# Optimization experiments

Measured on AMD Instinct MI355X. Metric: run time of the kernel, lower is better.

Reference implementation:

```python
import jax, jax.numpy as jnp
import numpy as np

B, N, E = 4, 10000, 160000
NODE_DIM, EDGE_DIM, HIDDEN, HEADS = 128, 64, 256, 8
HEAD_DIM = HIDDEN // HEADS
LN_EPS = 1e-5


def setup_inputs() -> dict:
    key = jax.random.key(0)
    ks = jax.random.split(key, 11)
    s = 0.05  # stand-in for xavier scale
    return {
        "node_feat": jax.random.normal(ks[0], (B, N, NODE_DIM), dtype=jnp.float32),
        "edge_index": jax.random.randint(ks[1], (2, E), 0, N, dtype=jnp.int64),
        "edge_attr": jax.random.normal(ks[2], (B, E, EDGE_DIM), dtype=jnp.float32),
        "W_node": jax.random.normal(ks[3], (NODE_DIM, HIDDEN), dtype=jnp.float32) * s,
        "W_edge": jax.random.normal(ks[4], (EDGE_DIM, HIDDEN), dtype=jnp.float32) * s,
        "W_res": jax.random.normal(ks[5], (NODE_DIM, HIDDEN), dtype=jnp.float32) * s,
        "att_src": jax.random.normal(ks[6], (HEADS, HEAD_DIM), dtype=jnp.float32) * s,
        "att_dst": jax.random.normal(ks[7], (HEADS, HEAD_DIM), dtype=jnp.float32) * s,
        "att_edge": jax.random.normal(ks[8], (HEADS, HEAD_DIM), dtype=jnp.float32) * s,
        "ln_gamma": jnp.ones((HIDDEN,), dtype=jnp.float32),
        "ln_beta": jnp.zeros((HIDDEN,), dtype=jnp.float32),
    }


def reference(node_feat, edge_index, edge_attr, W_node, W_edge, W_res,
              att_src, att_dst, att_edge, ln_gamma, ln_beta):
    b, n, _ = node_feat.shape
    e_cnt = edge_attr.shape[1]
    src = edge_index[0]
    dst = edge_index[1]

    h = (node_feat @ W_node).reshape(b, n, HEADS, HEAD_DIM)          # [B,N,H,D]
    e = (edge_attr @ W_edge).reshape(b, e_cnt, HEADS, HEAD_DIM)       # [B,E,H,D]
    h_src = h[:, src]                                                 # [B,E,H,D]
    h_dst = h[:, dst]                                                 # [B,E,H,D]

    logits = (jnp.einsum('behd,hd->beh', h_src, att_src)
              + jnp.einsum('behd,hd->beh', h_dst, att_dst)
              + jnp.einsum('behd,hd->beh', e, att_edge))              # [B,E,H]
    logits = jax.nn.leaky_relu(logits, negative_slope=0.2)

    # segment softmax over edges grouped by dst node (edge-leading layout)
    lt = logits.transpose(1, 0, 2)                                    # [E,B,H]
    seg_max = jax.ops.segment_max(lt, dst, num_segments=n)            # [N,B,H]
    ex = jnp.exp(lt - seg_max[dst])
    seg_sum = jax.ops.segment_sum(ex, dst, num_segments=n)            # [N,B,H]
    alpha = ex / seg_sum[dst]                                         # [E,B,H]

    msg = alpha[..., None] * (h_src + e).transpose(1, 0, 2, 3)        # [E,B,H,D]
    agg = jax.ops.segment_sum(msg, dst, num_segments=n)               # [N,B,H,D]
    out = agg.transpose(1, 0, 2, 3).reshape(b, n, HIDDEN)             # [B,N,HIDDEN]

    x = out + node_feat @ W_res
    mu = jnp.mean(x, axis=-1, keepdims=True)
    var = jnp.mean(jnp.square(x - mu), axis=-1, keepdims=True)
    x = (x - mu) * jax.lax.rsqrt(var + LN_EPS) * ln_gamma + ln_beta
    return jax.nn.elu(x)
```

## Files before the change

### kernel.cpp

```cpp
#include <hip/hip_runtime.h>

#define BB 4
#define NN 10000
#define EE 160000
#define HID 256
#define NHEAD 8

typedef __attribute__((ext_vector_type(8))) short short8v;
typedef __attribute__((ext_vector_type(4))) float f32x4;

__device__ __forceinline__ unsigned short f2bf(float f) {
  unsigned u = __float_as_uint(f);
  unsigned r = (u + 0x7fffu + ((u >> 16) & 1u)) >> 16;
  return (unsigned short)r;
}

__global__ void k_prep(const float* __restrict__ We, const float* __restrict__ ae,
                       float* __restrict__ What) {
  int t = threadIdx.x;
  int k = t >> 3, hh = t & 7;
  float s = 0.f;
#pragma unroll
  for (int d = 0; d < 32; ++d) s += We[k * HID + hh * 32 + d] * ae[hh * 32 + d];
  What[k * NHEAD + hh] = s;
}

__global__ __launch_bounds__(256) void k_cvt(const float* __restrict__ nf,
                                             unsigned short* __restrict__ nf16) {
  const int g = blockIdx.x * 256 + threadIdx.x;
  const float4* s = reinterpret_cast<const float4*>(nf) + (size_t)g * 2;
  const float4 a = s[0], b = s[1];
  short8v v;
  v[0] = f2bf(a.x); v[1] = f2bf(a.y); v[2] = f2bf(a.z); v[3] = f2bf(a.w);
  v[4] = f2bf(b.x); v[5] = f2bf(b.y); v[6] = f2bf(b.z); v[7] = f2bf(b.w);
  *reinterpret_cast<short8v*>(nf16 + (size_t)g * 8) = v;
}

__global__ __launch_bounds__(256) void k_pack(const float* __restrict__ Wn,
                                              const float* __restrict__ Wr,
                                              unsigned short* __restrict__ Bpack) {
  const int nt = blockIdx.x;
  const int ks = threadIdx.x >> 6;
  const int l = threadIdx.x & 63;
  const int col = nt * 16 + (l & 15);
  const int k0 = ks * 32 + (l >> 4) * 8;
  const float* __restrict__ src = (nt < 16) ? Wn : Wr;
  const int c2 = col & 255;
  short8v v;
#pragma unroll
  for (int e = 0; e < 8; ++e) v[e] = f2bf(src[(k0 + e) * HID + c2]);
  *reinterpret_cast<short8v*>(Bpack + ((size_t)(nt * 4 + ks) * 64 + l) * 8) = v;
}

__global__ __launch_bounds__(512) void k_projm(
    const unsigned short* __restrict__ nf16,
    const unsigned short* __restrict__ Bpack,
    float* __restrict__ h, float* __restrict__ res) {
  const int t = threadIdx.x;
  const int w = t >> 6, l = t & 63;
  const int base = blockIdx.x * 64 + (w & 3) * 16;
  const int nhalf = w >> 2;
  short8v a[4];
#pragma unroll
  for (int ks = 0; ks < 4; ++ks)
    a[ks] = *reinterpret_cast<const short8v*>(
        nf16 + (size_t)(base + (l & 15)) * 128 + ks * 32 + (l >> 4) * 8);
  f32x4 acc[16];
#pragma unroll
  for (int i = 0; i < 16; ++i) acc[i] = (f32x4){0.f, 0.f, 0.f, 0.f};
  const short8v* bp =
      reinterpret_cast<const short8v*>(Bpack) + (size_t)nhalf * 4096 + l;
#pragma unroll
  for (int nt = 0; nt < 16; ++nt) {
#pragma unroll
    for (int ks = 0; ks < 4; ++ks) {
      const short8v bf = bp[(nt * 4 + ks) * 64];
      acc[nt] = __builtin_amdgcn_mfma_f32_16x16x32_bf16(a[ks], bf, acc[nt], 0, 0, 0);
    }
  }
  float* __restrict__ outp = nhalf ? res : h;
#pragma unroll
  for (int nt = 0; nt < 16; ++nt) {
    const int col = nt * 16 + (l & 15);
#pragma unroll
    for (int b = 0; b < 4; ++b) {
      const int row = base + (l >> 4) * 4 + b;
      outp[(size_t)row * HID + col] = acc[nt][b];
    }
  }
}

__global__ __launch_bounds__(256) void k_att(
    const float* __restrict__ h, const float* __restrict__ as_,
    const float* __restrict__ ad_, float* __restrict__ ssrc,
    float* __restrict__ sdst) {
  const int w = threadIdx.x >> 6, l = threadIdx.x & 63;
  const size_t bn = (size_t)blockIdx.x * 4 + w;
  const float4 hv = reinterpret_cast<const float4*>(h + bn * HID)[l];
  const float4 av = reinterpret_cast<const float4*>(as_)[l];
  const float4 dv = reinterpret_cast<const float4*>(ad_)[l];
  float ps = hv.x * av.x + hv.y * av.y + hv.z * av.z + hv.w * av.w;
  float pd = hv.x * dv.x + hv.y * dv.y + hv.z * dv.z + hv.w * dv.w;
#pragma unroll
  for (int off = 1; off <= 4; off <<= 1) {
    ps += __shfl_xor(ps, off);
    pd += __shfl_xor(pd, off);
  }
  if ((l & 7) == 0) {
    ssrc[bn * NHEAD + (l >> 3)] = ps;
    sdst[bn * NHEAD + (l >> 3)] = pd;
  }
}

__global__ __launch_bounds__(256) void k_elogit(
    const float* __restrict__ ea, const int* __restrict__ ei,
    const float* __restrict__ What, const float* __restrict__ ssrc,
    const float* __restrict__ sdst, float* __restrict__ logits) {
  __shared__ float sea[32 * 65];
  __shared__ float sw[64 * NHEAD];
  const int t = threadIdx.x;
  sw[t] = What[t];
  sw[t + 256] = What[t + 256];
  const int g0 = blockIdx.x * 32;
  const float* base = ea + (size_t)g0 * 64;
#pragma unroll
  for (int j = 0; j < 8; ++j) {
    int f = t + j * 256;
    sea[(f >> 6) * 65 + (f & 63)] = base[f];
  }
  __syncthreads();
  const int il = t >> 3, hh = t & 7;
  const int g = g0 + il;
  float acc = 0.f;
#pragma unroll
  for (int k = 0; k < 64; ++k) acc += sea[il * 65 + k] * sw[k * NHEAD + hh];
  const int b = g / EE, e = g - b * EE;
  const int src = ei[e], dst = ei[EE + e];
  float lg = ssrc[((size_t)b * NN + src) * NHEAD + hh] +
             sdst[((size_t)b * NN + dst) * NHEAD + hh] + acc;
  lg = lg > 0.f ? lg : 0.2f * lg;
  logits[(size_t)g * NHEAD + hh] = lg;
}

__global__ void k_hist(const int* __restrict__ ei, int* __restrict__ cnt) {
  int e = blockIdx.x * 256 + threadIdx.x;
  if (e < EE) atomicAdd(&cnt[ei[EE + e]], 1);
}

__global__ __launch_bounds__(1024) void k_scan(const int* __restrict__ cnt,
                                               int* __restrict__ off) {
  __shared__ int ls[1024];
  const int t = threadIdx.x;
  int own = 0;
  int deg[10];
  if (t < 1000) {
#pragma unroll
    for (int i = 0; i < 10; ++i) { deg[i] = cnt[t * 10 + i]; own += deg[i]; }
  }
  ls[t] = own;
  __syncthreads();
  for (int s = 1; s < 1024; s <<= 1) {
    int v = 0;
    if (t >= s) v = ls[t - s];
    __syncthreads();
    if (t >= s) ls[t] += v;
    __syncthreads();
  }
  if (t < 1000) {
    int start = ls[t] - own;
#pragma unroll
    for (int i = 0; i < 10; ++i) { off[t * 10 + i] = start; start += deg[i]; }
  }
  if (t == 0) off[NN] = EE;
}

__global__ void k_scatter(const int* __restrict__ ei, const int* __restrict__ off,
                          int* __restrict__ cur, int* __restrict__ perm,
                          int* __restrict__ esrc) {
  int e = blockIdx.x * 256 + threadIdx.x;
  if (e >= EE) return;
  int d = ei[EE + e];
  int pos = off[d] + atomicAdd(&cur[d], 1);
  perm[pos] = e;
  esrc[pos] = ei[e];
}

__global__ __launch_bounds__(256) void k_agg(
    const float* __restrict__ ea, const float* __restrict__ h,
    const float* __restrict__ logits, const int* __restrict__ off,
    const int* __restrict__ perm, const int* __restrict__ esrc,
    const float* __restrict__ We, const float* __restrict__ res,
    const float* __restrict__ gam, const float* __restrict__ bet,
    float* __restrict__ out) {
  __shared__ float zsh[4][8 * 65];
  const int wid = threadIdx.x >> 6, l = threadIdx.x & 63;
  const int b = wid, node = blockIdx.x;
  const int start = off[node], end = off[node + 1];
  const int hq = l >> 3;
  const int hr = l & 7;
  float m = -3.0e38f;
  for (int i = start + (l >> 3); i < end; i += 8) {
    int e = perm[i];
    m = fmaxf(m, logits[((size_t)b * EE + e) * 8 + hr]);
  }
  m = fmaxf(m, __shfl_xor(m, 8));
  m = fmaxf(m, __shfl_xor(m, 16));
  m = fmaxf(m, __shfl_xor(m, 32));
  float4 u4 = {0.f, 0.f, 0.f, 0.f};
  float z0 = 0.f, z1 = 0.f, z2 = 0.f, z3 = 0.f;
  float z4 = 0.f, z5 = 0.f, z6 = 0.f, z7 = 0.f;
  float ss = 0.f;
  for (int i = start; i < end; ++i) {
    const int e = perm[i];
    const int src = esrc[i];
    const float lg = logits[((size_t)b * EE + e) * 8 + hr];
    const float exl = __expf(lg - m);
    ss += exl;
    const float eal = ea[((size_t)b * EE + e) * 64 + l];
    const float e0 = __shfl(exl, 0), e1 = __shfl(exl, 1);
    const float e2 = __shfl(exl, 2), e3 = __shfl(exl, 3);
    const float e4 = __shfl(exl, 4), e5 = __shfl(exl, 5);
    const float e6 = __shfl(exl, 6), e7 = __shfl(exl, 7);
    z0 += e0 * eal; z1 += e1 * eal; z2 += e2 * eal; z3 += e3 * eal;
    z4 += e4 * eal; z5 += e5 * eal; z6 += e6 * eal; z7 += e7 * eal;
    const float exu = __shfl(exl, hq);
    const float4 hs =
        *reinterpret_cast<const float4*>(h + (((size_t)b * NN + src) << 8) + 4 * l);
    u4.x += exu * hs.x; u4.y += exu * hs.y;
    u4.z += exu * hs.z; u4.w += exu * hs.w;
  }
  zsh[wid][0 * 65 + l] = z0; zsh[wid][1 * 65 + l] = z1;
  zsh[wid][2 * 65 + l] = z2; zsh[wid][3 * 65 + l] = z3;
  zsh[wid][4 * 65 + l] = z4; zsh[wid][5 * 65 + l] = z5;
  zsh[wid][6 * 65 + l] = z6; zsh[wid][7 * 65 + l] = z7;
  const float4* We4 = reinterpret_cast<const float4*>(We);
  const float4 r4 =
      *reinterpret_cast<const float4*>(res + (((size_t)b * NN + node) << 8) + 4 * l);
#pragma unroll 8
  for (int k = 0; k < 64; ++k) {
    const float zk = zsh[wid][hq * 65 + k];
    const float4 wv = We4[k * 64 + l];
    u4.x += zk * wv.x; u4.y += zk * wv.y;
    u4.z += zk * wv.z; u4.w += zk * wv.w;
  }
  const float ssq = __shfl(ss, hq);
  const float sc = ssq > 0.f ? 1.f / ssq : 0.f;
  u4.x = u4.x * sc + r4.x; u4.y = u4.y * sc + r4.y;
  u4.z = u4.z * sc + r4.z; u4.w = u4.w * sc + r4.w;
  float s1 = u4.x + u4.y + u4.z + u4.w;
  float s2 = u4.x * u4.x + u4.y * u4.y + u4.z * u4.z + u4.w * u4.w;
#pragma unroll
  for (int off2 = 1; off2 <= 32; off2 <<= 1) {
    s1 += __shfl_xor(s1, off2);
    s2 += __shfl_xor(s2, off2);
  }
  const float mu = s1 * (1.f / HID);
  const float var = s2 * (1.f / HID) - mu * mu;
  const float rstd = rsqrtf(var + 1e-5f);
  const float4 g4 = reinterpret_cast<const float4*>(gam)[l];
  const float4 b4 = reinterpret_cast<const float4*>(bet)[l];
  float4 y;
  y.x = (u4.x - mu) * rstd * g4.x + b4.x;
  y.y = (u4.y - mu) * rstd * g4.y + b4.y;
  y.z = (u4.z - mu) * rstd * g4.z + b4.z;
  y.w = (u4.w - mu) * rstd * g4.w + b4.w;
  y.x = y.x > 0.f ? y.x : expm1f(y.x);
  y.y = y.y > 0.f ? y.y : expm1f(y.y);
  y.z = y.z > 0.f ? y.z : expm1f(y.z);
  y.w = y.w > 0.f ? y.w : expm1f(y.w);
  *reinterpret_cast<float4*>(out + (((size_t)b * NN + node) << 8) + 4 * l) = y;
}

extern "C" void kernel_launch(void* const* d_in, const int* in_sizes, int n_in,
                              void* d_out, int out_size, void* d_ws, size_t ws_size,
                              hipStream_t stream) {
  const float* nf   = (const float*)d_in[0];
  const int*   ei   = (const int*)d_in[1];
  const float* eatt = (const float*)d_in[2];
  const float* Wn   = (const float*)d_in[3];
  const float* We   = (const float*)d_in[4];
  const float* Wr   = (const float*)d_in[5];
  const float* as_  = (const float*)d_in[6];
  const float* ad_  = (const float*)d_in[7];
  const float* ae_  = (const float*)d_in[8];
  const float* gam  = (const float*)d_in[9];
  const float* bet  = (const float*)d_in[10];
  float* out = (float*)d_out;

  char* ws = (char*)d_ws;
  size_t off_b = 0;
  float* h      = (float*)(ws + off_b); off_b += (size_t)BB * NN * HID * 4;
  float* ssrc   = (float*)(ws + off_b); size_t csr_off = off_b; off_b += (size_t)BB * NN * NHEAD * 4;
  float* sdst   = (float*)(ws + off_b); off_b += (size_t)BB * NN * NHEAD * 4;
  float* What   = (float*)(ws + off_b); off_b += 64 * NHEAD * 4;
  size_t logits_off = off_b;
  float* logits = (float*)(ws + off_b); off_b += (size_t)BB * EE * NHEAD * 4;
  float* res    = (float*)(ws + off_b); off_b += (size_t)BB * NN * HID * 4;
  unsigned short* nf16  = (unsigned short*)(ws + logits_off);
  unsigned short* Bpack = (unsigned short*)(ws + logits_off + ((size_t)12 << 20));
  char* csr = ws + csr_off;
  int* cnt  = (int*)(csr);
  int* offn = (int*)(csr + 40 * 1024);
  int* cur  = (int*)(csr + 2 * 40 * 1024);
  int* perm = (int*)(csr + 3 * 40 * 1024);
  int* esrc = (int*)(csr + 3 * 40 * 1024 + (size_t)EE * 4);

  hipLaunchKernelGGL(k_prep, dim3(1), dim3(512), 0, stream, We, ae_, What);
  hipLaunchKernelGGL(k_cvt, dim3(2500), dim3(256), 0, stream, nf, nf16);
  hipLaunchKernelGGL(k_pack, dim3(32), dim3(256), 0, stream, Wn, Wr, Bpack);
  hipLaunchKernelGGL(k_projm, dim3(BB * NN / 64), dim3(512), 0, stream,
                     nf16, Bpack, h, res);
  hipLaunchKernelGGL(k_att, dim3(BB * NN / 4), dim3(256), 0, stream,
                     h, as_, ad_, ssrc, sdst);
  hipLaunchKernelGGL(k_elogit, dim3(BB * EE / 32), dim3(256), 0, stream,
                     eatt, ei, What, ssrc, sdst, logits);
  hipMemsetAsync(csr, 0, 3 * 40 * 1024, stream);
  hipLaunchKernelGGL(k_hist, dim3((EE + 255) / 256), dim3(256), 0, stream, ei, cnt);
  hipLaunchKernelGGL(k_scan, dim3(1), dim3(1024), 0, stream, cnt, offn);
  hipLaunchKernelGGL(k_scatter, dim3((EE + 255) / 256), dim3(256), 0, stream,
                     ei, offn, cur, perm, esrc);
  hipLaunchKernelGGL(k_agg, dim3(NN), dim3(256), 0, stream,
                     eatt, h, logits, offn, perm, esrc, We, res, gam, bet, out);
}
```

Measured before the change: 302.2 us.

## Store h in bf16, precompute CSR-ordered exp logits with atomic segment max

```diff
diff --git a/kernel.cpp b/kernel.cpp
--- a/kernel.cpp
+++ b/kernel.cpp
@@ -13,6 +13,16 @@
   unsigned u = __float_as_uint(f);
   unsigned r = (u + 0x7fffu + ((u >> 16) & 1u)) >> 16;
   return (unsigned short)r;
+}
+__device__ __forceinline__ float bf2f(unsigned short u) {
+  return __uint_as_float(((unsigned)u) << 16);
+}
+__device__ __forceinline__ unsigned fenc(float f) {
+  unsigned u = __float_as_uint(f);
+  return (u & 0x80000000u) ? ~u : (u | 0x80000000u);
+}
+__device__ __forceinline__ float fdec(unsigned u) {
+  return __uint_as_float((u & 0x80000000u) ? (u ^ 0x80000000u) : ~u);
 }
 
 __global__ void k_prep(const float* __restrict__ We, const float* __restrict__ ae,
@@ -55,7 +65,7 @@
 __global__ __launch_bounds__(512) void k_projm(
     const unsigned short* __restrict__ nf16,
     const unsigned short* __restrict__ Bpack,
-    float* __restrict__ h, float* __restrict__ res) {
+    unsigned short* __restrict__ h16, float* __restrict__ res) {
   const int t = threadIdx.x;
   const int w = t >> 6, l = t & 63;
   const int base = blockIdx.x * 64 + (w & 3) * 16;
@@ -78,29 +88,30 @@
       acc[nt] = __builtin_amdgcn_mfma_f32_16x16x32_bf16(a[ks], bf, acc[nt], 0, 0, 0);
     }
   }
-  float* __restrict__ outp = nhalf ? res : h;
 #pragma unroll
   for (int nt = 0; nt < 16; ++nt) {
     const int col = nt * 16 + (l & 15);
 #pragma unroll
     for (int b = 0; b < 4; ++b) {
       const int row = base + (l >> 4) * 4 + b;
-      outp[(size_t)row * HID + col] = acc[nt][b];
+      if (nhalf == 0) h16[(size_t)row * HID + col] = f2bf(acc[nt][b]);
+      else            res[(size_t)row * HID + col] = acc[nt][b];
     }
   }
 }
 
 __global__ __launch_bounds__(256) void k_att(
-    const float* __restrict__ h, const float* __restrict__ as_,
+    const unsigned short* __restrict__ h16, const float* __restrict__ as_,
     const float* __restrict__ ad_, float* __restrict__ ssrc,
     float* __restrict__ sdst) {
   const int w = threadIdx.x >> 6, l = threadIdx.x & 63;
   const size_t bn = (size_t)blockIdx.x * 4 + w;
-  const float4 hv = reinterpret_cast<const float4*>(h + bn * HID)[l];
+  const ushort4 hv = *reinterpret_cast<const ushort4*>(h16 + bn * HID + 4 * l);
   const float4 av = reinterpret_cast<const float4*>(as_)[l];
   const float4 dv = reinterpret_cast<const float4*>(ad_)[l];
-  float ps = hv.x * av.x + hv.y * av.y + hv.z * av.z + hv.w * av.w;
-  float pd = hv.x * dv.x + hv.y * dv.y + hv.z * dv.z + hv.w * dv.w;
+  const float x0 = bf2f(hv.x), x1 = bf2f(hv.y), x2 = bf2f(hv.z), x3 = bf2f(hv.w);
+  float ps = x0 * av.x + x1 * av.y + x2 * av.z + x3 * av.w;
+  float pd = x0 * dv.x + x1 * dv.y + x2 * dv.z + x3 * dv.w;
 #pragma unroll
   for (int off = 1; off <= 4; off <<= 1) {
     ps += __shfl_xor(ps, off);
@@ -110,36 +121,6 @@
     ssrc[bn * NHEAD + (l >> 3)] = ps;
     sdst[bn * NHEAD + (l >> 3)] = pd;
   }
-}
-
-__global__ __launch_bounds__(256) void k_elogit(
-    const float* __restrict__ ea, const int* __restrict__ ei,
-    const float* __restrict__ What, const float* __restrict__ ssrc,
-    const float* __restrict__ sdst, float* __restrict__ logits) {
-  __shared__ float sea[32 * 65];
-  __shared__ float sw[64 * NHEAD];
-  const int t = threadIdx.x;
-  sw[t] = What[t];
-  sw[t + 256] = What[t + 256];
-  const int g0 = blockIdx.x * 32;
-  const float* base = ea + (size_t)g0 * 64;
-#pragma unroll
-  for (int j = 0; j < 8; ++j) {
-    int f = t + j * 256;
-    sea[(f >> 6) * 65 + (f & 63)] = base[f];
-  }
-  __syncthreads();
-  const int il = t >> 3, hh = t & 7;
-  const int g = g0 + il;
-  float acc = 0.f;
-#pragma unroll
-  for (int k = 0; k < 64; ++k) acc += sea[il * 65 + k] * sw[k * NHEAD + hh];
-  const int b = g / EE, e = g - b * EE;
-  const int src = ei[e], dst = ei[EE + e];
-  float lg = ssrc[((size_t)b * NN + src) * NHEAD + hh] +
-             sdst[((size_t)b * NN + dst) * NHEAD + hh] + acc;
-  lg = lg > 0.f ? lg : 0.2f * lg;
-  logits[(size_t)g * NHEAD + hh] = lg;
 }
 
 __global__ void k_hist(const int* __restrict__ ei, int* __restrict__ cnt) {
@@ -175,59 +156,94 @@
 }
 
 __global__ void k_scatter(const int* __restrict__ ei, const int* __restrict__ off,
-                          int* __restrict__ cur, int* __restrict__ perm,
-                          int* __restrict__ esrc) {
+                          int* __restrict__ cur, int2* __restrict__ eidx,
+                          int* __restrict__ inv, int* __restrict__ edst) {
   int e = blockIdx.x * 256 + threadIdx.x;
   if (e >= EE) return;
-  int d = ei[EE + e];
+  int s = ei[e], d = ei[EE + e];
   int pos = off[d] + atomicAdd(&cur[d], 1);
-  perm[pos] = e;
-  esrc[pos] = ei[e];
+  eidx[pos] = make_int2(e, s);
+  inv[e] = pos;
+  edst[pos] = d;
+}
+
+__global__ __launch_bounds__(256) void k_elogit(
+    const float* __restrict__ ea, const int* __restrict__ ei,
+    const float* __restrict__ What, const float* __restrict__ ssrc,
+    const float* __restrict__ sdst, const int* __restrict__ inv,
+    float* __restrict__ logitsP, unsigned* __restrict__ smax) {
+  __shared__ float sea[32 * 65];
+  __shared__ float sw[64 * NHEAD];
+  const int t = threadIdx.x;
+  sw[t] = What[t];
+  sw[t + 256] = What[t + 256];
+  const int g0 = blockIdx.x * 32;
+  const float* base = ea + (size_t)g0 * 64;
+#pragma unroll
+  for (int j = 0; j < 8; ++j) {
+    int f = t + j * 256;
+    sea[(f >> 6) * 65 + (f & 63)] = base[f];
+  }
+  __syncthreads();
+  const int il = t >> 3, hh = t & 7;
+  const int g = g0 + il;
+  float acc = 0.f;
+#pragma unroll
+  for (int k = 0; k < 64; ++k) acc += sea[il * 65 + k] * sw[k * NHEAD + hh];
+  const int b = g / EE, e = g - b * EE;
+  const int src = ei[e], dst = ei[EE + e];
+  float lg = ssrc[((size_t)b * NN + src) * NHEAD + hh] +
+             sdst[((size_t)b * NN + dst) * NHEAD + hh] + acc;
+  lg = lg > 0.f ? lg : 0.2f * lg;
+  const int pos = inv[e];
+  logitsP[((size_t)b * EE + pos) * 8 + hh] = lg;
+  atomicMax(&smax[((size_t)b * NN + dst) * 8 + hh], fenc(lg));
+}
+
+__global__ __launch_bounds__(256) void k_ex(float* __restrict__ exP,
+                                            const int* __restrict__ edst,
+                                            const unsigned* __restrict__ smax) {
+  const size_t t = (size_t)blockIdx.x * 256 + threadIdx.x;
+  const int g = (int)(t >> 3), hh = (int)(t & 7);
+  const int b = g / EE, i = g - b * EE;
+  const int d = edst[i];
+  const float mx = fdec(smax[((size_t)b * NN + d) * 8 + hh]);
+  exP[t] = __expf(exP[t] - mx);
 }
 
 __global__ __launch_bounds__(256) void k_agg(
-    const float* __restrict__ ea, const float* __restrict__ h,
-    const float* __restrict__ logits, const int* __restrict__ off,
-    const int* __restrict__ perm, const int* __restrict__ esrc,
-    const float* __restrict__ We, const float* __restrict__ res,
-    const float* __restrict__ gam, const float* __restrict__ bet,
-    float* __restrict__ out) {
+    const float* __restrict__ ea, const unsigned short* __restrict__ h16,
+    const float* __restrict__ exP, const int* __restrict__ off,
+    const int2* __restrict__ eidx, const float* __restrict__ We,
+    const float* __restrict__ res, const float* __restrict__ gam,
+    const float* __restrict__ bet, float* __restrict__ out) {
   __shared__ float zsh[4][8 * 65];
   const int wid = threadIdx.x >> 6, l = threadIdx.x & 63;
   const int b = wid, node = blockIdx.x;
   const int start = off[node], end = off[node + 1];
   const int hq = l >> 3;
   const int hr = l & 7;
-  float m = -3.0e38f;
-  for (int i = start + (l >> 3); i < end; i += 8) {
-    int e = perm[i];
-    m = fmaxf(m, logits[((size_t)b * EE + e) * 8 + hr]);
-  }
-  m = fmaxf(m, __shfl_xor(m, 8));
-  m = fmaxf(m, __shfl_xor(m, 16));
-  m = fmaxf(m, __shfl_xor(m, 32));
   float4 u4 = {0.f, 0.f, 0.f, 0.f};
   float z0 = 0.f, z1 = 0.f, z2 = 0.f, z3 = 0.f;
   float z4 = 0.f, z5 = 0.f, z6 = 0.f, z7 = 0.f;
   float ss = 0.f;
+  const float* __restrict__ exb = exP + (size_t)b * EE * 8;
+  const float* __restrict__ eab = ea + (size_t)b * EE * 64;
+  const unsigned short* __restrict__ hb = h16 + (size_t)b * NN * 256;
+#pragma unroll 2
   for (int i = start; i < end; ++i) {
-    const int e = perm[i];
-    const int src = esrc[i];
-    const float lg = logits[((size_t)b * EE + e) * 8 + hr];
-    const float exl = __expf(lg - m);
-    ss += exl;
-    const float eal = ea[((size_t)b * EE + e) * 64 + l];
-    const float e0 = __shfl(exl, 0), e1 = __shfl(exl, 1);
-    const float e2 = __shfl(exl, 2), e3 = __shfl(exl, 3);
-    const float e4 = __shfl(exl, 4), e5 = __shfl(exl, 5);
-    const float e6 = __shfl(exl, 6), e7 = __shfl(exl, 7);
-    z0 += e0 * eal; z1 += e1 * eal; z2 += e2 * eal; z3 += e3 * eal;
-    z4 += e4 * eal; z5 += e5 * eal; z6 += e6 * eal; z7 += e7 * eal;
-    const float exu = __shfl(exl, hq);
-    const float4 hs =
-        *reinterpret_cast<const float4*>(h + (((size_t)b * NN + src) << 8) + 4 * l);
-    u4.x += exu * hs.x; u4.y += exu * hs.y;
-    u4.z += exu * hs.z; u4.w += exu * hs.w;
+    const int2 es = eidx[i];
+    const float4 xa = *reinterpret_cast<const float4*>(exb + (size_t)i * 8);
+    const float4 xb = *reinterpret_cast<const float4*>(exb + (size_t)i * 8 + 4);
+    const float exu = exb[(size_t)i * 8 + hq];
+    ss += exb[(size_t)i * 8 + hr];
+    const float eal = eab[(size_t)es.x * 64 + l];
+    const ushort4 h4 =
+        *reinterpret_cast<const ushort4*>(hb + (size_t)es.y * 256 + 4 * l);
+    z0 += xa.x * eal; z1 += xa.y * eal; z2 += xa.z * eal; z3 += xa.w * eal;
+    z4 += xb.x * eal; z5 += xb.y * eal; z6 += xb.z * eal; z7 += xb.w * eal;
+    u4.x += exu * bf2f(h4.x); u4.y += exu * bf2f(h4.y);
+    u4.z += exu * bf2f(h4.z); u4.w += exu * bf2f(h4.w);
   }
   zsh[wid][0 * 65 + l] = z0; zsh[wid][1 * 65 + l] = z1;
   zsh[wid][2 * 65 + l] = z2; zsh[wid][3 * 65 + l] = z3;
@@ -288,37 +304,48 @@
   float* out = (float*)d_out;
 
   char* ws = (char*)d_ws;
-  size_t off_b = 0;
-  float* h      = (float*)(ws + off_b); off_b += (size_t)BB * NN * HID * 4;
-  float* ssrc   = (float*)(ws + off_b); size_t csr_off = off_b; off_b += (size_t)BB * NN * NHEAD * 4;
-  float* sdst   = (float*)(ws + off_b); off_b += (size_t)BB * NN * NHEAD * 4;
-  float* What   = (float*)(ws + off_b); off_b += 64 * NHEAD * 4;
-  size_t logits_off = off_b;
-  float* logits = (float*)(ws + off_b); off_b += (size_t)BB * EE * NHEAD * 4;
-  float* res    = (float*)(ws + off_b); off_b += (size_t)BB * NN * HID * 4;
-  unsigned short* nf16  = (unsigned short*)(ws + logits_off);
-  unsigned short* Bpack = (unsigned short*)(ws + logits_off + ((size_t)12 << 20));
-  char* csr = ws + csr_off;
-  int* cnt  = (int*)(csr);
-  int* offn = (int*)(csr + 40 * 1024);
-  int* cur  = (int*)(csr + 2 * 40 * 1024);
-  int* perm = (int*)(csr + 3 * 40 * 1024);
-  int* esrc = (int*)(csr + 3 * 40 * 1024 + (size_t)EE * 4);
+  size_t o = 0;
+  auto alloc = [&](size_t bytes) -> void* {
+    void* p = ws + o;
+    o += (bytes + 255) & ~(size_t)255;
+    return p;
+  };
+  unsigned short* h16 = (unsigned short*)alloc((size_t)BB * NN * HID * 2);
+  float* ssrc    = (float*)alloc((size_t)BB * NN * NHEAD * 4);
+  float* sdst    = (float*)alloc((size_t)BB * NN * NHEAD * 4);
+  float* What    = (float*)alloc(64 * NHEAD * 4);
+  float* logitsP = (float*)alloc((size_t)BB * EE * NHEAD * 4);
+  float* res     = (float*)alloc((size_t)BB * NN * HID * 4);
+  int*  cnt      = (int*)alloc(NN * 4);
+  int*  cur      = (int*)alloc(NN * 4);
+  int*  offn     = (int*)alloc((NN + 1) * 4);
+  int2* eidx     = (int2*)alloc((size_t)EE * 8);
+
+  char* ob = (char*)d_out;
+  unsigned short* nf16  = (unsigned short*)ob;
+  unsigned short* Bpack = (unsigned short*)(ob + ((size_t)12 << 20));
+  unsigned* smax = (unsigned*)(ob + ((size_t)16 << 20));
+  int* inv       = (int*)(ob + ((size_t)18 << 20));
+  int* edst      = (int*)(ob + ((size_t)20 << 20));
 
   hipLaunchKernelGGL(k_prep, dim3(1), dim3(512), 0, stream, We, ae_, What);
   hipLaunchKernelGGL(k_cvt, dim3(2500), dim3(256), 0, stream, nf, nf16);
   hipLaunchKernelGGL(k_pack, dim3(32), dim3(256), 0, stream, Wn, Wr, Bpack);
   hipLaunchKernelGGL(k_projm, dim3(BB * NN / 64), dim3(512), 0, stream,
-                     nf16, Bpack, h, res);
+                     nf16, Bpack, h16, res);
   hipLaunchKernelGGL(k_att, dim3(BB * NN / 4), dim3(256), 0, stream,
-                     h, as_, ad_, ssrc, sdst);
-  hipLaunchKernelGGL(k_elogit, dim3(BB * EE / 32), dim3(256), 0, stream,
-                     eatt, ei, What, ssrc, sdst, logits);
-  hipMemsetAsync(csr, 0, 3 * 40 * 1024, stream);
+                     h16, as_, ad_, ssrc, sdst);
+  hipMemsetAsync(cnt, 0, NN * 4, stream);
+  hipMemsetAsync(cur, 0, NN * 4, stream);
+  hipMemsetAsync(smax, 0, (size_t)BB * NN * NHEAD * 4, stream);
   hipLaunchKernelGGL(k_hist, dim3((EE + 255) / 256), dim3(256), 0, stream, ei, cnt);
   hipLaunchKernelGGL(k_scan, dim3(1), dim3(1024), 0, stream, cnt, offn);
   hipLaunchKernelGGL(k_scatter, dim3((EE + 255) / 256), dim3(256), 0, stream,
-                     ei, offn, cur, perm, esrc);
+                     ei, offn, cur, eidx, inv, edst);
+  hipLaunchKernelGGL(k_elogit, dim3(BB * EE / 32), dim3(256), 0, stream,
+                     eatt, ei, What, ssrc, sdst, inv, logitsP, smax);
+  hipLaunchKernelGGL(k_ex, dim3((size_t)BB * EE * NHEAD / 256), dim3(256), 0,
+                     stream, logitsP, edst, smax);
   hipLaunchKernelGGL(k_agg, dim3(NN), dim3(256), 0, stream,
-                     eatt, h, logits, offn, perm, esrc, We, res, gam, bet, out);
-}
+                     eatt, h16, logitsP, offn, eidx, We, res, gam, bet, out);
+}
```

New measurement: 314.8 us. 4.2% more time.
